# Performance work log

Hardware: AMD Instinct MI355X
Metric: run time of the kernel (lower is better)

The kernel has to match this reference:

```python
import jax, jax.numpy as jnp
import numpy as np

N_NODES = 100000
N_EDGES = 3200000
NUM_FEATURES = 512
LATENT_DIM = 64
HIDDEN = 2 * LATENT_DIM


def gcn_conv(x, src, dst, deg_inv_sqrt, W, b, n_nodes):
    # GCNConv: out = D^{-1/2} (A+I) D^{-1/2} X W + b  (transform first, then aggregate)
    h = x @ W  # [N, out]
    norm = deg_inv_sqrt[src] * deg_inv_sqrt[dst]  # [E]
    msg = h[src] * norm[:, None]  # gather + scale
    out = jax.ops.segment_sum(msg, dst, num_segments=n_nodes)
    return out + b


def setup_inputs() -> dict:
    key = jax.random.key(0)
    ks = jax.random.split(key, 8)
    features = jax.random.normal(ks[0], (N_NODES, NUM_FEATURES), dtype=jnp.float32)
    edge_index = jax.random.randint(ks[1], (2, N_EDGES), 0, N_NODES, dtype=jnp.int64)
    # Glorot-ish params
    W1 = jax.random.normal(ks[2], (NUM_FEATURES, HIDDEN), dtype=jnp.float32) / np.sqrt(NUM_FEATURES)
    b1 = jnp.zeros((HIDDEN,), dtype=jnp.float32)
    Wm = jax.random.normal(ks[3], (HIDDEN, LATENT_DIM), dtype=jnp.float32) / np.sqrt(HIDDEN)
    bm = jnp.zeros((LATENT_DIM,), dtype=jnp.float32)
    Wv = jax.random.normal(ks[4], (HIDDEN, LATENT_DIM), dtype=jnp.float32) / np.sqrt(HIDDEN)
    bv = jnp.zeros((LATENT_DIM,), dtype=jnp.float32)
    return {"features": features, "edge_index": edge_index,
            "W1": W1, "b1": b1, "Wm": Wm, "bm": bm, "Wv": Wv, "bv": bv}


def reference(features, edge_index, W1, b1, Wm, bm, Wv, bv):
    n = features.shape[0]
    loop = jnp.arange(n, dtype=edge_index.dtype)
    src = jnp.concatenate([edge_index[0], loop])  # add self-loops
    dst = jnp.concatenate([edge_index[1], loop])
    deg = jax.ops.segment_sum(jnp.ones_like(dst, dtype=features.dtype), dst, num_segments=n)
    deg_inv_sqrt = jnp.where(deg > 0, jax.lax.rsqrt(deg), 0.0)

    h = jax.nn.relu(gcn_conv(features, src, dst, deg_inv_sqrt, W1, b1, n))
    mean = gcn_conv(h, src, dst, deg_inv_sqrt, Wm, bm, n)
    var = gcn_conv(h, src, dst, deg_inv_sqrt, Wv, bv, n)
    return (mean, var)
```

## Files before the change

kernel.cpp:

```cpp
#include <hip/hip_runtime.h>

#define N_FEAT 512
#define HID 128
#define LAT 64

#define NB 98
#define BSHIFT 10
#define BS 1024
#define CAP 34816
#define CHUNK 4096

__device__ __forceinline__ unsigned short f2bf(float f) {
    unsigned u = __float_as_uint(f);
    return (unsigned short)((u + 0x7FFFu + ((u >> 16) & 1u)) >> 16);
}
__device__ __forceinline__ float bf2f(unsigned short h) {
    return __uint_as_float(((unsigned)h) << 16);
}

typedef __attribute__((ext_vector_type(8))) short bf16x8;
typedef __attribute__((ext_vector_type(4))) float f32x4;
typedef __attribute__((ext_vector_type(8))) unsigned short u16x8;

__global__ __launch_bounds__(256) void bin_kernel(const int* __restrict__ src,
                                                  const int* __restrict__ dst,
                                                  int* __restrict__ gcursor,
                                                  uint2* __restrict__ binned, int E) {
    __shared__ int hist[NB];
    __shared__ int basel[NB];
    __shared__ int gbase[NB];
    __shared__ int cursor[NB];
    __shared__ uint2 staged[CHUNK];
    int tid = threadIdx.x;
    int e0 = blockIdx.x * CHUNK;
    int nE = min(CHUNK, E - e0);
    if (nE <= 0) return;
    for (int i = tid; i < NB; i += 256) hist[i] = 0;
    __syncthreads();
    for (int i = tid; i < nE; i += 256) {
        int d = dst[e0 + i];
        atomicAdd(&hist[d >> BSHIFT], 1);
    }
    __syncthreads();
    if (tid < NB) basel[tid] = hist[tid];
    __syncthreads();
    for (int off = 1; off < NB; off <<= 1) {
        int x = (tid >= off && tid < NB) ? basel[tid - off] : 0;
        __syncthreads();
        if (tid < NB) basel[tid] += x;
        __syncthreads();
    }
    if (tid < NB) {
        int c = hist[tid];
        basel[tid] -= c;
        gbase[tid] = (c > 0) ? atomicAdd(&gcursor[tid], c) : 0;
        cursor[tid] = basel[tid];
    }
    __syncthreads();
    for (int i = tid; i < nE; i += 256) {
        int s = src[e0 + i];
        int d = dst[e0 + i];
        int b = d >> BSHIFT;
        int pos = atomicAdd(&cursor[b], 1);
        staged[pos] = make_uint2((unsigned)s, (unsigned)d);
    }
    __syncthreads();
    for (int i = tid; i < nE; i += 256) {
        uint2 e = staged[i];
        int b = (int)(e.y >> BSHIFT);
        int ofs = gbase[b] + (i - basel[b]);
        if (ofs < CAP) binned[(size_t)b * CAP + ofs] = e;
    }
}

__global__ __launch_bounds__(1024) void build_a_kernel(const uint2* __restrict__ binned,
                                                       const int* __restrict__ gcursor,
                                                       int* __restrict__ counts,
                                                       float* __restrict__ dis,
                                                       int* __restrict__ offsets, int N) {
    __shared__ int nh[BS];
    __shared__ int pref[BS];
    int b = blockIdx.x;
    int tid = threadIdx.x;
    int nEdges = min(gcursor[b], CAP);
    const uint2* rgn = binned + (size_t)b * CAP;
    nh[tid] = 0;
    __syncthreads();
    for (int i = tid; i < nEdges; i += 1024)
        atomicAdd(&nh[rgn[i].y & (BS - 1)], 1);
    __syncthreads();
    int v = nh[tid];
    pref[tid] = v;
    __syncthreads();
    for (int off = 1; off < BS; off <<= 1) {
        int x = (tid >= off) ? pref[tid - off] : 0;
        __syncthreads();
        pref[tid] += x;
        __syncthreads();
    }
    int excl = pref[tid] - v;
    int node = (b << BSHIFT) + tid;
    if (node < N) {
        counts[node] = v;
        dis[node] = rsqrtf((float)(v + 1));
        offsets[node] = b * CAP + excl;
    }
}

__global__ __launch_bounds__(1024) void build_b_kernel(const uint2* __restrict__ binned,
                                                       const int* __restrict__ gcursor,
                                                       const int* __restrict__ offsets,
                                                       const float* __restrict__ dis,
                                                       int2* __restrict__ pairs, int N) {
    __shared__ int cur[BS];
    int b = blockIdx.x;
    int tid = threadIdx.x;
    int nEdges = min(gcursor[b], CAP);
    const uint2* rgn = binned + (size_t)b * CAP;
    int node = (b << BSHIFT) + tid;
    cur[tid] = (node < N) ? offsets[node] : 0;
    __syncthreads();
    for (int i = tid; i < nEdges; i += 1024) {
        uint2 e = rgn[i];
        int pos = atomicAdd(&cur[e.y & (BS - 1)], 1);
        float ws = dis[e.x];
        pairs[pos] = make_int2((int)e.x, __float_as_int(ws));
    }
}

__global__ __launch_bounds__(256) void wsplit_kernel(const float* __restrict__ W,
                                                     unsigned short* __restrict__ WhT,
                                                     unsigned short* __restrict__ WlT) {
    int i = blockIdx.x * 256 + threadIdx.x;
    if (i >= N_FEAT * HID) return;
    int k = i >> 7;
    int n = i & 127;
    float w = W[i];
    unsigned short h = f2bf(w);
    float r = w - bf2f(h);
    WhT[(size_t)n * N_FEAT + k] = h;
    WlT[(size_t)n * N_FEAT + k] = f2bf(r);
}

__global__ __launch_bounds__(256) void wsplit2_kernel(const float* __restrict__ Wm,
                                                      const float* __restrict__ Wv,
                                                      unsigned short* __restrict__ WhT2,
                                                      unsigned short* __restrict__ WlT2) {
    int i = blockIdx.x * 256 + threadIdx.x;
    if (i >= HID * HID) return;
    int k = i >> 7;
    int n = i & 127;
    float w = (n < 64) ? Wm[(size_t)k * LAT + n] : Wv[(size_t)k * LAT + (n - 64)];
    unsigned short h = f2bf(w);
    float r = w - bf2f(h);
    WhT2[(size_t)n * HID + k] = h;
    WlT2[(size_t)n * HID + k] = f2bf(r);
}

#define GM 128
#define GK 32
#define LDA 40

__global__ __launch_bounds__(256) void gemm1_mfma(const float* __restrict__ X,
                                                  const unsigned short* __restrict__ WhT,
                                                  const unsigned short* __restrict__ WlT,
                                                  unsigned short* __restrict__ Tb, int M) {
    __shared__ unsigned short Ah[GM][LDA];
    __shared__ unsigned short Al[GM][LDA];
    __shared__ unsigned short Bh[HID][LDA];
    __shared__ unsigned short Bl[HID][LDA];

    int tid = threadIdx.x;
    int row = tid >> 1;
    int c0 = (tid & 1) * 16;

    int row_g = blockIdx.x * GM + row;
    if (row_g > M - 1) row_g = M - 1;
    const float* xbase = X + (size_t)row_g * N_FEAT;
    const unsigned short* whb = WhT + (size_t)row * N_FEAT;
    const unsigned short* wlb = WlT + (size_t)row * N_FEAT;

    int wid = tid >> 6, lane = tid & 63;
    int wm = wid >> 1, wn = wid & 1;
    int lm = lane & 15;
    int lk8 = (lane >> 4) * 8;

    f32x4 acc[4][4];
    #pragma unroll
    for (int i = 0; i < 4; ++i)
        #pragma unroll
        for (int j = 0; j < 4; ++j) acc[i][j] = (f32x4){0.f, 0.f, 0.f, 0.f};

    float4 xv0 = *(const float4*)(xbase + c0);
    float4 xv1 = *(const float4*)(xbase + c0 + 4);
    float4 xv2 = *(const float4*)(xbase + c0 + 8);
    float4 xv3 = *(const float4*)(xbase + c0 + 12);
    uint4 bhv0 = *(const uint4*)(whb + c0);
    uint4 bhv1 = *(const uint4*)(whb + c0 + 8);
    uint4 blv0 = *(const uint4*)(wlb + c0);
    uint4 blv1 = *(const uint4*)(wlb + c0 + 8);

    for (int k0 = 0; k0 < N_FEAT; k0 += GK) {
        __syncthreads();
        {
            float xs[16] = {xv0.x, xv0.y, xv0.z, xv0.w, xv1.x, xv1.y, xv1.z, xv1.w,
                            xv2.x, xv2.y, xv2.z, xv2.w, xv3.x, xv3.y, xv3.z, xv3.w};
            unsigned short* arow = &Ah[row][c0];
            unsigned short* lrow = &Al[row][c0];
            #pragma unroll
            for (int j = 0; j < 16; j += 2) {
                unsigned short h0 = f2bf(xs[j]);
                unsigned short h1 = f2bf(xs[j + 1]);
                float r0 = xs[j] - bf2f(h0);
                float r1 = xs[j + 1] - bf2f(h1);
                *(unsigned*)&arow[j] = (unsigned)h0 | ((unsigned)h1 << 16);
                *(unsigned*)&lrow[j] = (unsigned)f2bf(r0) | ((unsigned)f2bf(r1) << 16);
            }
            *(uint4*)&Bh[row][c0]     = bhv0;
            *(uint4*)&Bh[row][c0 + 8] = bhv1;
            *(uint4*)&Bl[row][c0]     = blv0;
            *(uint4*)&Bl[row][c0 + 8] = blv1;
        }
        __syncthreads();
        if (k0 + GK < N_FEAT) {
            const float* xp = xbase + k0 + GK + c0;
            xv0 = *(const float4*)(xp);
            xv1 = *(const float4*)(xp + 4);
            xv2 = *(const float4*)(xp + 8);
            xv3 = *(const float4*)(xp + 12);
            bhv0 = *(const uint4*)(whb + k0 + GK + c0);
            bhv1 = *(const uint4*)(whb + k0 + GK + c0 + 8);
            blv0 = *(const uint4*)(wlb + k0 + GK + c0);
            blv1 = *(const uint4*)(wlb + k0 + GK + c0 + 8);
        }
        bf16x8 ah[4], al[4], bh[4], bl[4];
        #pragma unroll
        for (int i = 0; i < 4; ++i) {
            ah[i] = *(const bf16x8*)&Ah[wm * 64 + i * 16 + lm][lk8];
            al[i] = *(const bf16x8*)&Al[wm * 64 + i * 16 + lm][lk8];
            bh[i] = *(const bf16x8*)&Bh[wn * 64 + i * 16 + lm][lk8];
            bl[i] = *(const bf16x8*)&Bl[wn * 64 + i * 16 + lm][lk8];
        }
        #pragma unroll
        for (int i = 0; i < 4; ++i)
            #pragma unroll
            for (int j = 0; j < 4; ++j) {
                acc[i][j] = __builtin_amdgcn_mfma_f32_16x16x32_bf16(ah[i], bh[j], acc[i][j], 0, 0, 0);
                acc[i][j] = __builtin_amdgcn_mfma_f32_16x16x32_bf16(al[i], bh[j], acc[i][j], 0, 0, 0);
                acc[i][j] = __builtin_amdgcn_mfma_f32_16x16x32_bf16(ah[i], bl[j], acc[i][j], 0, 0, 0);
            }
    }

    int orow0 = blockIdx.x * GM + wm * 64 + (lane >> 4) * 4;
    int ocol0 = wn * 64 + lm;
    #pragma unroll
    for (int i = 0; i < 4; ++i)
        #pragma unroll
        for (int j = 0; j < 4; ++j)
            #pragma unroll
            for (int r = 0; r < 4; ++r) {
                int orow = orow0 + i * 16 + r;
                if (orow < M)
                    Tb[(size_t)orow * HID + ocol0 + j * 16] = f2bf(acc[i][j][r]);
            }
}

__global__ __launch_bounds__(256) void gemm2_mfma(const unsigned short* __restrict__ Gh,
                                                  const unsigned short* __restrict__ Gl,
                                                  const unsigned short* __restrict__ WhT2,
                                                  const unsigned short* __restrict__ WlT2,
                                                  const float* __restrict__ bm,
                                                  const float* __restrict__ bv,
                                                  float* __restrict__ outm,
                                                  float* __restrict__ outv, int M) {
    __shared__ unsigned short Ah[GM][LDA];
    __shared__ unsigned short Al[GM][LDA];
    __shared__ unsigned short Bh[HID][LDA];
    __shared__ unsigned short Bl[HID][LDA];

    int tid = threadIdx.x;
    int row = tid >> 1;
    int c0 = (tid & 1) * 16;

    int row_g = blockIdx.x * GM + row;
    if (row_g > M - 1) row_g = M - 1;
    const unsigned short* ghb = Gh + (size_t)row_g * HID;
    const unsigned short* glb = Gl + (size_t)row_g * HID;
    const unsigned short* whb = WhT2 + (size_t)row * HID;
    const unsigned short* wlb = WlT2 + (size_t)row * HID;

    int wid = tid >> 6, lane = tid & 63;
    int wm = wid >> 1, wn = wid & 1;
    int lm = lane & 15;
    int lk8 = (lane >> 4) * 8;

    f32x4 acc[4][4];
    #pragma unroll
    for (int i = 0; i < 4; ++i)
        #pragma unroll
        for (int j = 0; j < 4; ++j) acc[i][j] = (f32x4){0.f, 0.f, 0.f, 0.f};

    uint4 ahv0 = *(const uint4*)(ghb + c0);
    uint4 ahv1 = *(const uint4*)(ghb + c0 + 8);
    uint4 alv0 = *(const uint4*)(glb + c0);
    uint4 alv1 = *(const uint4*)(glb + c0 + 8);
    uint4 bhv0 = *(const uint4*)(whb + c0);
    uint4 bhv1 = *(const uint4*)(whb + c0 + 8);
    uint4 blv0 = *(const uint4*)(wlb + c0);
    uint4 blv1 = *(const uint4*)(wlb + c0 + 8);

    for (int k0 = 0; k0 < HID; k0 += GK) {
        __syncthreads();
        *(uint4*)&Ah[row][c0]     = ahv0;
        *(uint4*)&Ah[row][c0 + 8] = ahv1;
        *(uint4*)&Al[row][c0]     = alv0;
        *(uint4*)&Al[row][c0 + 8] = alv1;
        *(uint4*)&Bh[row][c0]     = bhv0;
        *(uint4*)&Bh[row][c0 + 8] = bhv1;
        *(uint4*)&Bl[row][c0]     = blv0;
        *(uint4*)&Bl[row][c0 + 8] = blv1;
        __syncthreads();
        if (k0 + GK < HID) {
            ahv0 = *(const uint4*)(ghb + k0 + GK + c0);
            ahv1 = *(const uint4*)(ghb + k0 + GK + c0 + 8);
            alv0 = *(const uint4*)(glb + k0 + GK + c0);
            alv1 = *(const uint4*)(glb + k0 + GK + c0 + 8);
            bhv0 = *(const uint4*)(whb + k0 + GK + c0);
            bhv1 = *(const uint4*)(whb + k0 + GK + c0 + 8);
            blv0 = *(const uint4*)(wlb + k0 + GK + c0);
            blv1 = *(const uint4*)(wlb + k0 + GK + c0 + 8);
        }
        bf16x8 ah[4], al[4], bh[4], bl[4];
        #pragma unroll
        for (int i = 0; i < 4; ++i) {
            ah[i] = *(const bf16x8*)&Ah[wm * 64 + i * 16 + lm][lk8];
            al[i] = *(const bf16x8*)&Al[wm * 64 + i * 16 + lm][lk8];
            bh[i] = *(const bf16x8*)&Bh[wn * 64 + i * 16 + lm][lk8];
            bl[i] = *(const bf16x8*)&Bl[wn * 64 + i * 16 + lm][lk8];
        }
        #pragma unroll
        for (int i = 0; i < 4; ++i)
            #pragma unroll
            for (int j = 0; j < 4; ++j) {
                acc[i][j] = __builtin_amdgcn_mfma_f32_16x16x32_bf16(ah[i], bh[j], acc[i][j], 0, 0, 0);
                acc[i][j] = __builtin_amdgcn_mfma_f32_16x16x32_bf16(al[i], bh[j], acc[i][j], 0, 0, 0);
                acc[i][j] = __builtin_amdgcn_mfma_f32_16x16x32_bf16(ah[i], bl[j], acc[i][j], 0, 0, 0);
            }
    }

    int orow0 = blockIdx.x * GM + wm * 64 + (lane >> 4) * 4;
    #pragma unroll
    for (int j = 0; j < 4; ++j) {
        int col = wn * 64 + j * 16 + lm;
        float bb = (col < 64) ? bm[col] : bv[col - 64];
        float* optr = (col < 64) ? (outm + col) : (outv + (col - 64));
        #pragma unroll
        for (int i = 0; i < 4; ++i)
            #pragma unroll
            for (int r = 0; r < 4; ++r) {
                int orow = orow0 + i * 16 + r;
                if (orow < M) optr[(size_t)orow * LAT] = acc[i][j][r] + bb;
            }
    }
}

template <bool RELU_BIAS, bool SPLIT_OUT>
__global__ __launch_bounds__(256) void agg_kernel(const unsigned short* __restrict__ Tb,
                                                  const int2* __restrict__ pairs,
                                                  const int* __restrict__ offsets,
                                                  const int* __restrict__ counts,
                                                  const float* __restrict__ dis,
                                                  const float* __restrict__ bias,
                                                  unsigned short* __restrict__ out_h,
                                                  unsigned short* __restrict__ out_l, int n) {
    int tid = threadIdx.x;
    int q = tid >> 4;
    int lane = tid & 15;
    int i = blockIdx.x * 16 + q;
    if (i >= n) return;
    float di = dis[i];
    int beg = offsets[i];
    int cnt = counts[i];
    const int2* ep = pairs + beg;
    u16x8 self = ((const u16x8*)(Tb + (size_t)i * HID))[lane];
    float acc[8];
    #pragma unroll
    for (int e = 0; e < 8; ++e) acc[e] = di * bf2f(self[e]);
    if (cnt > 0) {
        int cm1 = cnt - 1;
        int s[8]; float w[8];
        #pragma unroll
        for (int u = 0; u < 8; ++u) {
            int2 p = ep[min(u, cm1)];
            s[u] = p.x;
            w[u] = (u <= cm1) ? __int_as_float(p.y) : 0.f;
        }
        for (int j = 0; j < cnt; j += 8) {
            u16x8 v[8];
            #pragma unroll
            for (int u = 0; u < 8; ++u)
                v[u] = ((const u16x8*)(Tb + (size_t)s[u] * HID))[lane];
            int jn = j + 8;
            int sN[8]; float wN[8];
            #pragma unroll
            for (int u = 0; u < 8; ++u) {
                int2 p = ep[min(jn + u, cm1)];
                sN[u] = p.x;
                wN[u] = (jn + u <= cm1) ? __int_as_float(p.y) : 0.f;
            }
            #pragma unroll
            for (int u = 0; u < 8; ++u)
                #pragma unroll
                for (int e = 0; e < 8; ++e)
                    acc[e] += w[u] * bf2f(v[u][e]);
            #pragma unroll
            for (int u = 0; u < 8; ++u) { s[u] = sN[u]; w[u] = wN[u]; }
        }
    }
    #pragma unroll
    for (int e = 0; e < 8; ++e) acc[e] *= di;
    if (RELU_BIAS) {
        float4 bv0 = *(const float4*)(bias + lane * 8);
        float4 bv1 = *(const float4*)(bias + lane * 8 + 4);
        float bb[8] = {bv0.x, bv0.y, bv0.z, bv0.w, bv1.x, bv1.y, bv1.z, bv1.w};
        #pragma unroll
        for (int e = 0; e < 8; ++e) acc[e] = fmaxf(acc[e] + bb[e], 0.f);
    }
    if (!SPLIT_OUT) {
        u16x8 o;
        #pragma unroll
        for (int e = 0; e < 8; ++e) o[e] = f2bf(acc[e]);
        ((u16x8*)(out_h + (size_t)i * HID))[lane] = o;
    } else {
        u16x8 oh, ol;
        #pragma unroll
        for (int e = 0; e < 8; ++e) {
            unsigned short hh = f2bf(acc[e]);
            oh[e] = hh;
            ol[e] = f2bf(acc[e] - bf2f(hh));
        }
        ((u16x8*)(out_h + (size_t)i * HID))[lane] = oh;
        ((u16x8*)(out_l + (size_t)i * HID))[lane] = ol;
    }
}

extern "C" void kernel_launch(void* const* d_in, const int* in_sizes, int n_in,
                              void* d_out, int out_size, void* d_ws, size_t ws_size,
                              hipStream_t stream) {
    const float* X  = (const float*)d_in[0];
    const int* edge = (const int*)d_in[1];
    const float* W1 = (const float*)d_in[2];
    const float* b1 = (const float*)d_in[3];
    const float* Wm = (const float*)d_in[4];
    const float* bm = (const float*)d_in[5];
    const float* Wv = (const float*)d_in[6];
    const float* bv = (const float*)d_in[7];

    int N = in_sizes[0] / N_FEAT;
    int E = in_sizes[1] / 2;
    const int* srcp = edge;
    const int* dstp = edge + E;

    char* w = (char*)d_ws;
    size_t off = 0;
    auto alloc = [&](size_t bytes) -> void* {
        void* p = w + off;
        off = (off + bytes + 511) & ~(size_t)511;
        return p;
    };
    float* dis    = (float*)alloc((size_t)N * 4);
    int* counts   = (int*)alloc((size_t)N * 4);
    int* offsets  = (int*)alloc((size_t)N * 4);
    int* gcursor  = (int*)alloc((size_t)NB * 4);
    int2* pairs   = (int2*)alloc((size_t)NB * CAP * 8);
    unsigned short* tb = (unsigned short*)alloc((size_t)N * HID * 2);
    unsigned short* hb = (unsigned short*)alloc((size_t)N * HID * 2);
    unsigned short* whT = (unsigned short*)alloc((size_t)N_FEAT * HID * 2);
    unsigned short* wlT = (unsigned short*)alloc((size_t)N_FEAT * HID * 2);
    unsigned short* whT2 = (unsigned short*)alloc((size_t)HID * HID * 2);
    unsigned short* wlT2 = (unsigned short*)alloc((size_t)HID * HID * 2);
    unsigned short* gh = (unsigned short*)alloc((size_t)N * HID * 2);
    unsigned short* gl = (unsigned short*)alloc((size_t)N * HID * 2);
    uint2* binned = (uint2*)gh;

    hipMemsetAsync(gcursor, 0, (size_t)NB * 4, stream);
    int nChunks = (E + CHUNK - 1) / CHUNK;
    bin_kernel<<<nChunks, 256, 0, stream>>>(srcp, dstp, gcursor, binned, E);
    build_a_kernel<<<NB, 1024, 0, stream>>>(binned, gcursor, counts, dis, offsets, N);
    build_b_kernel<<<NB, 1024, 0, stream>>>(binned, gcursor, offsets, dis, pairs, N);

    wsplit_kernel<<<(N_FEAT * HID + 255) / 256, 256, 0, stream>>>(W1, whT, wlT);
    wsplit2_kernel<<<(HID * HID + 255) / 256, 256, 0, stream>>>(Wm, Wv, whT2, wlT2);
    gemm1_mfma<<<(N + GM - 1) / GM, 256, 0, stream>>>(X, whT, wlT, tb, N);
    agg_kernel<true, false><<<(N + 15) / 16, 256, 0, stream>>>(tb, pairs, offsets, counts, dis, b1, hb, nullptr, N);
    agg_kernel<false, true><<<(N + 15) / 16, 256, 0, stream>>>(hb, pairs, offsets, counts, dis, nullptr, gh, gl, N);

    float* outm = (float*)d_out;
    float* outv = outm + (size_t)N * LAT;
    gemm2_mfma<<<(N + GM - 1) / GM, 256, 0, stream>>>(gh, gl, whT2, wlT2, bm, bv, outm, outv, N);
}
```

Baseline: 735.2 us.

## Prescale rows by deg^-1/2 to drop per-edge weights; fuse CSR build kernels

The per-edge normalisation is factored out. GEMM1 output is prescaled by the source node's deg^-1/2, and the first aggregation also emits its output prescaled. The edge list therefore stores only source indices (4 bytes instead of 8), and the inner loop becomes a plain sum, with padding slots pointing at a zeroed dummy row N. The two CSR build kernels are merged into one, which saves a launch and a re-read of the binned edges, and the gather unroll grows from 8 to 12. The trade-off is slightly different bf16 rounding, because the scale is applied before quantisation, plus higher register pressure from the deeper unroll.

```diff
diff --git a/kernel.cpp b/kernel.cpp
--- a/kernel.cpp
+++ b/kernel.cpp
@@ -73,11 +73,12 @@
     }
 }
 
-__global__ __launch_bounds__(1024) void build_a_kernel(const uint2* __restrict__ binned,
-                                                       const int* __restrict__ gcursor,
-                                                       int* __restrict__ counts,
-                                                       float* __restrict__ dis,
-                                                       int* __restrict__ offsets, int N) {
+__global__ __launch_bounds__(1024) void build_kernel(const uint2* __restrict__ binned,
+                                                     const int* __restrict__ gcursor,
+                                                     int* __restrict__ counts,
+                                                     float* __restrict__ dis,
+                                                     int* __restrict__ offsets,
+                                                     int* __restrict__ pairs, int N) {
     __shared__ int nh[BS];
     __shared__ int pref[BS];
     int b = blockIdx.x;
@@ -105,26 +106,13 @@
         dis[node] = rsqrtf((float)(v + 1));
         offsets[node] = b * CAP + excl;
     }
-}
-
-__global__ __launch_bounds__(1024) void build_b_kernel(const uint2* __restrict__ binned,
-                                                       const int* __restrict__ gcursor,
-                                                       const int* __restrict__ offsets,
-                                                       const float* __restrict__ dis,
-                                                       int2* __restrict__ pairs, int N) {
-    __shared__ int cur[BS];
-    int b = blockIdx.x;
-    int tid = threadIdx.x;
-    int nEdges = min(gcursor[b], CAP);
-    const uint2* rgn = binned + (size_t)b * CAP;
-    int node = (b << BSHIFT) + tid;
-    cur[tid] = (node < N) ? offsets[node] : 0;
+    __syncthreads();
+    nh[tid] = b * CAP + excl;
     __syncthreads();
     for (int i = tid; i < nEdges; i += 1024) {
         uint2 e = rgn[i];
-        int pos = atomicAdd(&cur[e.y & (BS - 1)], 1);
-        float ws = dis[e.x];
-        pairs[pos] = make_int2((int)e.x, __float_as_int(ws));
+        int pos = atomicAdd(&nh[e.y & (BS - 1)], 1);
+        pairs[pos] = (int)e.x;
     }
 }
 
@@ -164,6 +152,7 @@
 __global__ __launch_bounds__(256) void gemm1_mfma(const float* __restrict__ X,
                                                   const unsigned short* __restrict__ WhT,
                                                   const unsigned short* __restrict__ WlT,
+                                                  const float* __restrict__ dis,
                                                   unsigned short* __restrict__ Tb, int M) {
     __shared__ unsigned short Ah[GM][LDA];
     __shared__ unsigned short Al[GM][LDA];
@@ -256,13 +245,15 @@
     #pragma unroll
     for (int i = 0; i < 4; ++i)
         #pragma unroll
-        for (int j = 0; j < 4; ++j)
-            #pragma unroll
-            for (int r = 0; r < 4; ++r) {
-                int orow = orow0 + i * 16 + r;
-                if (orow < M)
-                    Tb[(size_t)orow * HID + ocol0 + j * 16] = f2bf(acc[i][j][r]);
+        for (int r = 0; r < 4; ++r) {
+            int orow = orow0 + i * 16 + r;
+            if (orow < M) {
+                float dr = dis[orow];
+                #pragma unroll
+                for (int j = 0; j < 4; ++j)
+                    Tb[(size_t)orow * HID + ocol0 + j * 16] = f2bf(dr * acc[i][j][r]);
             }
+        }
 }
 
 __global__ __launch_bounds__(256) void gemm2_mfma(const unsigned short* __restrict__ Gh,
@@ -364,9 +355,10 @@
     }
 }
 
+#define AD 12
 template <bool RELU_BIAS, bool SPLIT_OUT>
 __global__ __launch_bounds__(256) void agg_kernel(const unsigned short* __restrict__ Tb,
-                                                  const int2* __restrict__ pairs,
+                                                  const int* __restrict__ pairs,
                                                   const int* __restrict__ offsets,
                                                   const int* __restrict__ counts,
                                                   const float* __restrict__ dis,
@@ -381,50 +373,48 @@
     float di = dis[i];
     int beg = offsets[i];
     int cnt = counts[i];
-    const int2* ep = pairs + beg;
+    const int* ep = pairs + beg;
     u16x8 self = ((const u16x8*)(Tb + (size_t)i * HID))[lane];
     float acc[8];
     #pragma unroll
-    for (int e = 0; e < 8; ++e) acc[e] = di * bf2f(self[e]);
+    for (int e = 0; e < 8; ++e) acc[e] = bf2f(self[e]);
     if (cnt > 0) {
         int cm1 = cnt - 1;
-        int s[8]; float w[8];
-        #pragma unroll
-        for (int u = 0; u < 8; ++u) {
-            int2 p = ep[min(u, cm1)];
-            s[u] = p.x;
-            w[u] = (u <= cm1) ? __int_as_float(p.y) : 0.f;
-        }
-        for (int j = 0; j < cnt; j += 8) {
-            u16x8 v[8];
-            #pragma unroll
-            for (int u = 0; u < 8; ++u)
+        int s[AD];
+        #pragma unroll
+        for (int u = 0; u < AD; ++u)
+            s[u] = (u <= cm1) ? ep[min(u, cm1)] : n;
+        for (int j = 0; j < cnt; j += AD) {
+            u16x8 v[AD];
+            #pragma unroll
+            for (int u = 0; u < AD; ++u)
                 v[u] = ((const u16x8*)(Tb + (size_t)s[u] * HID))[lane];
-            int jn = j + 8;
-            int sN[8]; float wN[8];
-            #pragma unroll
-            for (int u = 0; u < 8; ++u) {
-                int2 p = ep[min(jn + u, cm1)];
-                sN[u] = p.x;
-                wN[u] = (jn + u <= cm1) ? __int_as_float(p.y) : 0.f;
-            }
-            #pragma unroll
-            for (int u = 0; u < 8; ++u)
+            int jn = j + AD;
+            int sN[AD];
+            #pragma unroll
+            for (int u = 0; u < AD; ++u)
+                sN[u] = (jn + u <= cm1) ? ep[min(jn + u, cm1)] : n;
+            #pragma unroll
+            for (int u = 0; u < AD; ++u)
                 #pragma unroll
                 for (int e = 0; e < 8; ++e)
-                    acc[e] += w[u] * bf2f(v[u][e]);
-            #pragma unroll
-            for (int u = 0; u < 8; ++u) { s[u] = sN[u]; w[u] = wN[u]; }
-        }
-    }
-    #pragma unroll
-    for (int e = 0; e < 8; ++e) acc[e] *= di;
+                    acc[e] += bf2f(v[u][e]);
+            #pragma unroll
+            for (int u = 0; u < AD; ++u) s[u] = sN[u];
+        }
+    }
     if (RELU_BIAS) {
         float4 bv0 = *(const float4*)(bias + lane * 8);
         float4 bv1 = *(const float4*)(bias + lane * 8 + 4);
         float bb[8] = {bv0.x, bv0.y, bv0.z, bv0.w, bv1.x, bv1.y, bv1.z, bv1.w};
         #pragma unroll
-        for (int e = 0; e < 8; ++e) acc[e] = fmaxf(acc[e] + bb[e], 0.f);
+        for (int e = 0; e < 8; ++e) {
+            float t = fmaxf(di * acc[e] + bb[e], 0.f);
+            acc[e] = di * t;
+        }
+    } else {
+        #pragma unroll
+        for (int e = 0; e < 8; ++e) acc[e] *= di;
     }
     if (!SPLIT_OUT) {
         u16x8 o;
@@ -472,9 +462,9 @@
     int* counts   = (int*)alloc((size_t)N * 4);
     int* offsets  = (int*)alloc((size_t)N * 4);
     int* gcursor  = (int*)alloc((size_t)NB * 4);
-    int2* pairs   = (int2*)alloc((size_t)NB * CAP * 8);
-    unsigned short* tb = (unsigned short*)alloc((size_t)N * HID * 2);
-    unsigned short* hb = (unsigned short*)alloc((size_t)N * HID * 2);
+    int* pairs    = (int*)alloc((size_t)NB * CAP * 4);
+    unsigned short* tb = (unsigned short*)alloc((size_t)(N + 1) * HID * 2);
+    unsigned short* hb = (unsigned short*)alloc((size_t)(N + 1) * HID * 2);
     unsigned short* whT = (unsigned short*)alloc((size_t)N_FEAT * HID * 2);
     unsigned short* wlT = (unsigned short*)alloc((size_t)N_FEAT * HID * 2);
     unsigned short* whT2 = (unsigned short*)alloc((size_t)HID * HID * 2);
@@ -484,14 +474,15 @@
     uint2* binned = (uint2*)gh;
 
     hipMemsetAsync(gcursor, 0, (size_t)NB * 4, stream);
+    hipMemsetAsync(tb + (size_t)N * HID, 0, (size_t)HID * 2, stream);
+    hipMemsetAsync(hb + (size_t)N * HID, 0, (size_t)HID * 2, stream);
     int nChunks = (E + CHUNK - 1) / CHUNK;
     bin_kernel<<<nChunks, 256, 0, stream>>>(srcp, dstp, gcursor, binned, E);
-    build_a_kernel<<<NB, 1024, 0, stream>>>(binned, gcursor, counts, dis, offsets, N);
-    build_b_kernel<<<NB, 1024, 0, stream>>>(binned, gcursor, offsets, dis, pairs, N);
+    build_kernel<<<NB, 1024, 0, stream>>>(binned, gcursor, counts, dis, offsets, pairs, N);
 
     wsplit_kernel<<<(N_FEAT * HID + 255) / 256, 256, 0, stream>>>(W1, whT, wlT);
     wsplit2_kernel<<<(HID * HID + 255) / 256, 256, 0, stream>>>(Wm, Wv, whT2, wlT2);
-    gemm1_mfma<<<(N + GM - 1) / GM, 256, 0, stream>>>(X, whT, wlT, tb, N);
+    gemm1_mfma<<<(N + GM - 1) / GM, 256, 0, stream>>>(X, whT, wlT, dis, tb, N);
     agg_kernel<true, false><<<(N + 15) / 16, 256, 0, stream>>>(tb, pairs, offsets, counts, dis, b1, hb, nullptr, N);
     agg_kernel<false, true><<<(N + 15) / 16, 256, 0, stream>>>(hb, pairs, offsets, counts, dis, nullptr, gh, gl, N);
 
```

Result: faster. 687.6 us (-6.5%).
